# Performance work log

Hardware: AMD Instinct MI355X
Metric: run time of the kernel (lower is better)

Reference implementation:

```python
import jax, jax.numpy as jnp
import numpy as np

EPS = 1e-5      # numerical floor for degrees / std / attenuation
LEAK = 0.01     # LeakyReLU slope of mixing FCLayer
AVG_D = 3.3     # log(avg_degree + 1) from init_kwargs
BIG = 1e30      # masking constant for max/min aggregators


def setup_inputs() -> dict:
    key = jax.random.key(0)
    ks = jax.random.split(key, 12)
    B, N, Din, De, H = 8, 256, 128, 64, 128
    s = 0.05
    inp = {
        "input": jax.random.normal(ks[0], (B, N, Din), jnp.float32),
        "adj": (jax.random.uniform(ks[1], (B, N, N)) < 0.1).astype(jnp.float32),
        "adj_features": jax.random.normal(ks[2], (B, N, N, De), jnp.float32),
        "hidden": jnp.zeros((B * N, H), jnp.float32),
        "pre_W": jax.random.normal(ks[3], (2 * Din + De, Din), jnp.float32) * s,
        "pre_b": jnp.zeros((Din,), jnp.float32),
        "post_W": jax.random.normal(ks[4], (13 * Din, H), jnp.float32) * s,
        "post_b": jnp.zeros((H,), jnp.float32),
        "mix_W": jax.random.normal(ks[5], (H, H), jnp.float32) * s,
        "mix_b": jnp.zeros((H,), jnp.float32),
        "gru_Wih": jax.random.normal(ks[6], (3 * H, H), jnp.float32) * s,
        "gru_Whh": jax.random.normal(ks[7], (3 * H, H), jnp.float32) * s,
    }
    return inp


def reference(input, adj, adj_features, hidden, pre_W, pre_b, post_W, post_b,
              mix_W, mix_b, gru_Wih, gru_Whh):
    B, N, Din = input.shape
    H = mix_W.shape[1]
    # --- pretrans MLP over all pairs: Linear([h_i, h_j, e_ij]) ---
    # split the weight into blocks so we never materialize h_cat (B,N,N,2Din+De)
    Wi, Wj, We = pre_W[:Din], pre_W[Din:2 * Din], pre_W[2 * Din:]
    hi = input @ Wi            # (B,N,Din)
    hj = input @ Wj            # (B,N,Din)
    h_mod = (hi[:, :, None, :] + hj[:, None, :, :]
             + jnp.einsum('bije,ek->bijk', adj_features, We) + pre_b)  # (B,N,N,Din)
    # --- multi-aggregator masked reduction over source axis j ---
    deg = jnp.sum(adj, axis=2)                       # (B,N)
    degc = jnp.maximum(deg, EPS)[..., None]          # (B,N,1)
    s1 = jnp.einsum('bij,bijk->bik', adj, h_mod)
    s2 = jnp.einsum('bij,bijk->bik', adj, h_mod * h_mod)
    mean = s1 / degc
    var = jnp.maximum(s2 / degc - mean * mean, 0.0)
    std = jnp.sqrt(var + EPS)
    mask = adj[..., None] > 0
    has_nb = (deg > 0)[..., None]
    mx = jnp.where(has_nb, jnp.max(jnp.where(mask, h_mod, -BIG), axis=2), 0.0)
    mn = jnp.where(has_nb, jnp.min(jnp.where(mask, h_mod, BIG), axis=2), 0.0)
    m = jnp.concatenate([mean, mx, mn, std], axis=2)  # (B,N,4*Din)
    # --- scalers: identity, amplification, attenuation ---
    slog = (jnp.log(deg + 1.0) / AVG_D)[..., None]    # (B,N,1)
    m = jnp.concatenate([m, m * slog, m / (slog + EPS)], axis=2)  # (B,N,12*Din)
    # --- posttrans Linear + mixing FCLayer (LeakyReLU) ---
    m_cat = jnp.concatenate([input, m], axis=2)       # (B,N,13*Din)
    y = m_cat @ post_W + post_b                       # (B,N,H)
    y = y @ mix_W + mix_b
    y = jnp.where(y > 0, y, LEAK * y)
    # --- GRUCell (bias=False), torch gate order r,z,n ---
    x = y.reshape(B * N, H)
    gi = x @ gru_Wih.T
    gh = hidden @ gru_Whh.T
    r = jax.nn.sigmoid(gi[:, :H] + gh[:, :H])
    z = jax.nn.sigmoid(gi[:, H:2 * H] + gh[:, H:2 * H])
    n = jnp.tanh(gi[:, 2 * H:] + r * gh[:, 2 * H:])
    h_new = (1.0 - z) * n + z * hidden
    return h_new.reshape(B, N, H)
```

## Files before the change

kernel.cpp:

```cpp
#include <hip/hip_runtime.h>
#include <cstdint>
#include <cstddef>

#define EPSF 1e-5f
#define LEAKF 0.01f
#define AVGD 3.3f

static constexpr int Nn = 256, DIN = 128, DE = 64, Hn = 128;
static constexpr int BN = 2048;
static constexpr int CT = 1664;

typedef short bf16x8 __attribute__((ext_vector_type(8)));
typedef float f32x4  __attribute__((ext_vector_type(4)));
union BF8 { bf16x8 v; uint16_t u[8]; };

__device__ __forceinline__ float bf2f(uint16_t u) { return __uint_as_float(((uint32_t)u) << 16); }
__device__ __forceinline__ float bflo(uint32_t u)  { return __uint_as_float(u << 16); }
__device__ __forceinline__ uint16_t f2bf(float f) {
  uint32_t u = __float_as_uint(f);
  u += 0x7fffu + ((u >> 16) & 1u);
  return (uint16_t)(u >> 16);
}

__device__ __forceinline__ int detect_bf16(const uint32_t* w) {
  float lo = bflo(w[threadIdx.x & 63]);
  unsigned long long ok = __ballot(fabsf(lo) < 64.f);
  return ok == 0xFFFFFFFFFFFFFFFFull;
}
__device__ __forceinline__ float loadf(const void* p, size_t i, int isbf) {
  return isbf ? bf2f(((const uint16_t*)p)[i]) : ((const float*)p)[i];
}
__device__ __forceinline__ f32x4 mfma16(bf16x8 a, bf16x8 b, f32x4 c) {
  return __builtin_amdgcn_mfma_f32_16x16x32_bf16(a, b, c, 0, 0, 0);
}

__global__ __launch_bounds__(256) void k_prep(
    const void* __restrict__ input, const void* __restrict__ pre_W,
    const void* __restrict__ post_W, const void* __restrict__ mix_W,
    const void* __restrict__ Wih, const void* __restrict__ Whh,
    const void* __restrict__ hidden, const void* __restrict__ pre_b,
    uint16_t* __restrict__ preWTb, uint16_t* __restrict__ postTb,
    uint16_t* __restrict__ mixTb, uint16_t* __restrict__ Wihb,
    uint16_t* __restrict__ Whhb, uint16_t* __restrict__ hidb,
    uint16_t* __restrict__ Ab, float* __restrict__ hi, float* __restrict__ hj) {
  int isbf = detect_bf16((const uint32_t*)input);
  int b = blockIdx.x, tid = threadIdx.x;
  if (b < 264) {
    __shared__ float tile[32][33];
    const void* src; int R, C, t; uint16_t* bdst;
    if (b < 16)       { src = mix_W;  R = 128;  C = 128; t = b;       bdst = mixTb; }
    else if (b < 224) { src = post_W; R = 1664; C = 128; t = b - 16;  bdst = postTb; }
    else              { src = pre_W;  R = 320;  C = 128; t = b - 224; bdst = preWTb; }
    int bx = t & 3, by = t >> 2;
    int tx = tid & 31, ty = tid >> 5;
    int c0 = bx * 32, r0 = by * 32;
    #pragma unroll
    for (int dy = 0; dy < 32; dy += 8) {
      size_t idx = (size_t)(r0 + ty + dy) * C + (c0 + tx);
      tile[ty + dy][tx] = loadf(src, idx, isbf);
    }
    __syncthreads();
    #pragma unroll
    for (int dy = 0; dy < 32; dy += 8)
      bdst[(size_t)(c0 + ty + dy) * R + (r0 + tx)] = f2bf(tile[tx][ty + dy]);
  } else if (b < 440) {
    const void* src; uint16_t* dst; int base;
    if (b < 288)      { src = Wih;    dst = Wihb; base = (b - 264) * 2048; }
    else if (b < 312) { src = Whh;    dst = Whhb; base = (b - 288) * 2048; }
    else              { src = hidden; dst = hidb; base = (b - 312) * 2048; }
    int i = base + tid * 8;
    uint16_t v[8];
    if (isbf) *(uint4*)v = *(const uint4*)((const uint16_t*)src + i);
    else { const float* s = (const float*)src + i;
           #pragma unroll
           for (int e = 0; e < 8; e++) v[e] = f2bf(s[e]); }
    *(uint4*)(dst + i) = *(uint4*)v;
  } else if (b < 568) {
    int idx = (b - 440) * 2048 + tid * 8;
    int node = idx >> 7, col = idx & 127;
    uint16_t v[8];
    if (isbf) *(uint4*)v = *(const uint4*)((const uint16_t*)input + idx);
    else { const float* s = (const float*)input + idx;
           #pragma unroll
           for (int e = 0; e < 8; e++) v[e] = f2bf(s[e]); }
    *(uint4*)(Ab + (size_t)node * CT + col) = *(uint4*)v;
  } else {
    int lane = tid & 63, w = tid >> 6;
    int wg = (b - 568) * 4 + w;
    int rt = wg >> 4, nt = wg & 15;
    int ishj = nt >> 3, ct = nt & 7;
    int m16 = lane & 15, quad = lane >> 4;
    int col = ct * 16 + m16;
    int row = rt * 16 + m16;
    int kbase = ishj ? 128 : 0;
    f32x4 acc = {0.f, 0.f, 0.f, 0.f};
    #pragma unroll
    for (int kt = 0; kt < 4; kt++) {
      bf16x8 av;
      if (isbf) av = *(const bf16x8*)((const uint16_t*)input + (size_t)row * 128 + kt * 32 + quad * 8);
      else { const float* s = (const float*)input + (size_t)row * 128 + kt * 32 + quad * 8;
             BF8 t;
             #pragma unroll
             for (int e = 0; e < 8; e++) t.u[e] = f2bf(s[e]);
             av = t.v; }
      BF8 bb;
      #pragma unroll
      for (int j = 0; j < 8; j++) {
        size_t wi = (size_t)(kbase + kt * 32 + quad * 8 + j) * 128 + col;
        bb.u[j] = isbf ? ((const uint16_t*)pre_W)[wi] : f2bf(((const float*)pre_W)[wi]);
      }
      acc = mfma16(av, bb.v, acc);
    }
    float bias = ishj ? 0.f : loadf(pre_b, col, isbf);
    float* dst = ishj ? hj : hi;
    #pragma unroll
    for (int r = 0; r < 4; r++)
      dst[(size_t)(rt * 16 + quad * 4 + r) * 128 + col] = acc[r] + bias;
  }
}

__global__ __launch_bounds__(256) void k2_mfma(
    const void* __restrict__ input, const void* __restrict__ adj_raw,
    const void* __restrict__ af_raw,
    const float* __restrict__ hi, const float* __restrict__ hj,
    const uint16_t* __restrict__ preWTb, uint16_t* __restrict__ Ab) {
  __shared__ int nbr[Nn];
  __shared__ int wcnt[4];
  int isbf = detect_bf16((const uint32_t*)input);
  int bi = blockIdx.x, tid = threadIdx.x;
  int lane = tid & 63, w = tid >> 6;

  float a = loadf(adj_raw, (size_t)bi * Nn + tid, isbf);
  unsigned long long bm = __ballot(a > 0.f);
  int pre = __popcll(bm & ((1ull << lane) - 1ull));
  if (lane == 0) wcnt[w] = __popcll(bm);
  __syncthreads();
  int base = 0, cnt = 0;
  #pragma unroll
  for (int i = 0; i < 4; i++) { if (i < w) base += wcnt[i]; cnt += wcnt[i]; }
  if (a > 0.f) nbr[base + pre] = tid;
  __syncthreads();

  int m16 = lane & 15, quad = lane >> 4;
  int col0 = w * 32 + m16, col1 = col0 + 16;

  bf16x8 b00 = *(const bf16x8*)&preWTb[(size_t)col0 * 320 + 256 + quad * 8];
  bf16x8 b01 = *(const bf16x8*)&preWTb[(size_t)col0 * 320 + 288 + quad * 8];
  bf16x8 b10 = *(const bf16x8*)&preWTb[(size_t)col1 * 320 + 256 + quad * 8];
  bf16x8 b11 = *(const bf16x8*)&preWTb[(size_t)col1 * 320 + 288 + quad * 8];

  float base0 = hi[(size_t)bi * 128 + col0];
  float base1 = hi[(size_t)bi * 128 + col1];
  const float* hjb = &hj[(size_t)(bi & ~(Nn - 1)) * 128];

  float s1a = 0.f, s2a = 0.f, mxa = -1e30f, mna = 1e30f;
  float s1b = 0.f, s2b = 0.f, mxb = -1e30f, mnb = 1e30f;

  for (int ce = 0; ce < cnt; ce += 16) {
    int ei = ce + m16; if (ei >= cnt) ei = cnt - 1;
    int j = nbr[ei];
    bf16x8 a0, a1;
    if (isbf) {
      const uint16_t* ar = (const uint16_t*)af_raw + ((size_t)bi * Nn + j) * DE;
      a0 = *(const bf16x8*)(ar + quad * 8);
      a1 = *(const bf16x8*)(ar + 32 + quad * 8);
    } else {
      const float* ar = (const float*)af_raw + ((size_t)bi * Nn + j) * DE;
      BF8 t0, t1;
      #pragma unroll
      for (int e = 0; e < 8; e++) {
        t0.u[e] = f2bf(ar[quad * 8 + e]);
        t1.u[e] = f2bf(ar[32 + quad * 8 + e]);
      }
      a0 = t0.v; a1 = t1.v;
    }
    float hjv0[4], hjv1[4]; int vld[4];
    #pragma unroll
    for (int r = 0; r < 4; r++) {
      int e = ce + quad * 4 + r;
      vld[r] = (e < cnt);
      int jj = nbr[vld[r] ? e : (cnt - 1)];
      hjv0[r] = hjb[(size_t)jj * 128 + col0];
      hjv1[r] = hjb[(size_t)jj * 128 + col1];
    }
    f32x4 C0 = {0.f,0.f,0.f,0.f}, C1 = C0;
    C0 = mfma16(a0, b00, C0); C0 = mfma16(a1, b01, C0);
    C1 = mfma16(a0, b10, C1); C1 = mfma16(a1, b11, C1);
    #pragma unroll
    for (int r = 0; r < 4; r++) {
      float h0 = base0 + hjv0[r] + C0[r];
      float h1 = base1 + hjv1[r] + C1[r];
      if (vld[r]) {
        s1a += h0; s2a += h0 * h0; mxa = fmaxf(mxa, h0); mna = fminf(mna, h0);
        s1b += h1; s2b += h1 * h1; mxb = fmaxf(mxb, h1); mnb = fminf(mnb, h1);
      }
    }
  }
  #pragma unroll
  for (int off = 16; off <= 32; off <<= 1) {
    s1a += __shfl_xor(s1a, off); s2a += __shfl_xor(s2a, off);
    mxa = fmaxf(mxa, __shfl_xor(mxa, off)); mna = fminf(mna, __shfl_xor(mna, off));
    s1b += __shfl_xor(s1b, off); s2b += __shfl_xor(s2b, off);
    mxb = fmaxf(mxb, __shfl_xor(mxb, off)); mnb = fminf(mnb, __shfl_xor(mnb, off));
  }
  if (quad == 0) {
    float deg = (float)cnt, degc = fmaxf(deg, EPSF);
    float slog = logf(deg + 1.f) / AVGD;
    float inv  = 1.f / (slog + EPSF);
    uint16_t* mo = Ab + (size_t)bi * CT + 128;
    #pragma unroll
    for (int t = 0; t < 2; t++) {
      float s1 = t ? s1b : s1a, s2 = t ? s2b : s2a;
      float mx = t ? mxb : mxa, mn = t ? mnb : mna;
      int col = t ? col1 : col0;
      float mean = s1 / degc;
      float var  = fmaxf(s2 / degc - mean * mean, 0.f);
      float stdv = sqrtf(var + EPSF);
      if (cnt == 0) { mx = 0.f; mn = 0.f; }
      mo[0*128+col]  = f2bf(mean);        mo[1*128+col]  = f2bf(mx);
      mo[2*128+col]  = f2bf(mn);          mo[3*128+col]  = f2bf(stdv);
      mo[4*128+col]  = f2bf(mean * slog); mo[5*128+col]  = f2bf(mx * slog);
      mo[6*128+col]  = f2bf(mn * slog);   mo[7*128+col]  = f2bf(stdv * slog);
      mo[8*128+col]  = f2bf(mean * inv);  mo[9*128+col]  = f2bf(mx * inv);
      mo[10*128+col] = f2bf(mn * inv);    mo[11*128+col] = f2bf(stdv * inv);
    }
  }
}

__global__ __launch_bounds__(256) void k3a(
    const uint16_t* __restrict__ Ab, const uint16_t* __restrict__ postTb,
    const void* __restrict__ post_b, const void* __restrict__ input_flag,
    uint16_t* __restrict__ yb) {
  __shared__ float red[2][16][17];
  int isbf = detect_bf16((const uint32_t*)input_flag);
  int tid = threadIdx.x;
  int lane = tid & 63, w = tid >> 6;
  int wid = blockIdx.x * 4 + w;
  int tile = wid >> 1, kh = wid & 1, pair = w >> 1;
  int rt = tile >> 3, ct = tile & 7;
  int m16 = lane & 15, quad = lane >> 4;
  const uint16_t* ap = Ab     + (size_t)(rt * 16 + m16) * CT + kh * 832 + quad * 8;
  const uint16_t* bp = postTb + (size_t)(ct * 16 + m16) * CT + kh * 832 + quad * 8;
  f32x4 acc0 = {0.f,0.f,0.f,0.f}, acc1 = acc0;
  #pragma unroll 13
  for (int kt = 0; kt < 26; kt += 2) {
    acc0 = mfma16(*(const bf16x8*)(ap + kt * 32),      *(const bf16x8*)(bp + kt * 32),      acc0);
    acc1 = mfma16(*(const bf16x8*)(ap + kt * 32 + 32), *(const bf16x8*)(bp + kt * 32 + 32), acc1);
  }
  if (kh == 1) {
    #pragma unroll
    for (int r = 0; r < 4; r++) red[pair][quad * 4 + r][m16] = acc0[r] + acc1[r];
  }
  __syncthreads();
  if (kh == 0) {
    int col = ct * 16 + m16;
    float pb = loadf(post_b, col, isbf);
    #pragma unroll
    for (int r = 0; r < 4; r++)
      yb[(size_t)(rt * 16 + quad * 4 + r) * 128 + col] =
          f2bf(acc0[r] + acc1[r] + red[pair][quad * 4 + r][m16] + pb);
  }
}

__global__ __launch_bounds__(512) void k3b(
    const uint16_t* __restrict__ yb, const uint16_t* __restrict__ mixTb,
    const void* __restrict__ mix_b, const uint16_t* __restrict__ Wihb,
    const uint16_t* __restrict__ Whhb, const uint16_t* __restrict__ hidb,
    const void* __restrict__ input_flag, void* __restrict__ out) {
  constexpr int SX = 136;
  __shared__ __align__(16) uint16_t x_s[16 * SX];
  __shared__ __align__(16) uint16_t hid_s[16 * SX];
  int isbf = detect_bf16((const uint32_t*)input_flag);
  int tid = threadIdx.x;
  int n0 = blockIdx.x * 16;
  if (tid < 256) {
    int row = tid >> 4, c = (tid & 15) * 8;
    *(uint4*)&hid_s[row * SX + c] = *(const uint4*)&hidb[(size_t)(n0 + row) * 128 + c];
  }
  int lane = tid & 63, w = tid >> 6;
  int m16 = lane & 15, quad = lane >> 4;
  int col = w * 16 + m16;

  f32x4 acc = {0.f,0.f,0.f,0.f};
  const uint16_t* ya = yb    + (size_t)(n0 + m16) * 128 + quad * 8;
  const uint16_t* mb = mixTb + (size_t)col * 128 + quad * 8;
  #pragma unroll
  for (int kt = 0; kt < 4; kt++)
    acc = mfma16(*(const bf16x8*)(ya + kt * 32), *(const bf16x8*)(mb + kt * 32), acc);
  float mbias = loadf(mix_b, col, isbf);
  __syncthreads();
  #pragma unroll
  for (int r = 0; r < 4; r++) {
    float v = acc[r] + mbias; v = v > 0.f ? v : LEAKF * v;
    x_s[(quad * 4 + r) * SX + col] = f2bf(v);
  }
  __syncthreads();

  f32x4 gi[3], gh[3];
  #pragma unroll
  for (int q = 0; q < 3; q++) { gi[q] = {0.f,0.f,0.f,0.f}; gh[q] = {0.f,0.f,0.f,0.f}; }
  const uint16_t* xa = &x_s[m16 * SX + quad * 8];
  const uint16_t* ha = &hid_s[m16 * SX + quad * 8];
  #pragma unroll
  for (int kt = 0; kt < 4; kt++) {
    bf16x8 ax = *(const bf16x8*)(xa + kt * 32);
    bf16x8 ah = *(const bf16x8*)(ha + kt * 32);
    #pragma unroll
    for (int q = 0; q < 3; q++) {
      bf16x8 bi = *(const bf16x8*)&Wihb[(size_t)(q * 128 + col) * 128 + kt * 32 + quad * 8];
      bf16x8 bh = *(const bf16x8*)&Whhb[(size_t)(q * 128 + col) * 128 + kt * 32 + quad * 8];
      gi[q] = mfma16(ax, bi, gi[q]);
      gh[q] = mfma16(ah, bh, gh[q]);
    }
  }
  #pragma unroll
  for (int r = 0; r < 4; r++) {
    int row = quad * 4 + r;
    float rg = 1.f / (1.f + expf(-(gi[0][r] + gh[0][r])));
    float zg = 1.f / (1.f + expf(-(gi[1][r] + gh[1][r])));
    float ng = tanhf(gi[2][r] + rg * gh[2][r]);
    float hv = bf2f(hid_s[row * SX + col]);
    float res = (1.f - zg) * ng + zg * hv;
    size_t oi = (size_t)(n0 + row) * 128 + col;
    if (isbf) ((uint16_t*)out)[oi] = f2bf(res);
    else      ((float*)out)[oi]    = res;
  }
}

extern "C" void kernel_launch(void* const* d_in, const int* in_sizes, int n_in,
                              void* d_out, int out_size, void* d_ws, size_t ws_size,
                              hipStream_t stream) {
  const void* input  = d_in[0];
  const void* adj    = d_in[1];
  const void* af     = d_in[2];
  const void* hidden = d_in[3];
  const void* pre_W  = d_in[4];
  const void* pre_b  = d_in[5];
  const void* post_W = d_in[6];
  const void* post_b = d_in[7];
  const void* mix_W  = d_in[8];
  const void* mix_b  = d_in[9];
  const void* Wih    = d_in[10];
  const void* Whh    = d_in[11];

  float* ws = (float*)d_ws;
  float* hi = ws;
  float* hj = hi + 262144;
  uint16_t* Ab     = (uint16_t*)(hj + 262144);
  uint16_t* postTb = Ab + (size_t)BN * CT;
  uint16_t* mixTb  = postTb + 212992;
  uint16_t* preWTb = mixTb + 16384;
  uint16_t* Wihb   = preWTb + 40960;
  uint16_t* Whhb   = Wihb + 49152;
  uint16_t* hidb   = Whhb + 49152;
  uint16_t* yb     = hidb + 262144;

  k_prep<<<1080, 256, 0, stream>>>(input, pre_W, post_W, mix_W, Wih, Whh, hidden, pre_b,
                                   preWTb, postTb, mixTb, Wihb, Whhb, hidb, Ab, hi, hj);
  k2_mfma<<<BN, 256, 0, stream>>>(input, adj, af, hi, hj, preWTb, Ab);
  k3a<<<512, 256, 0, stream>>>(Ab, postTb, post_b, input, yb);
  k3b<<<128, 512, 0, stream>>>(yb, mixTb, mix_b, Wihb, Whhb, hidb, input, d_out);
}
```

Measured before the change: 236.0 us.

## Fold degree scalers into post-GEMM and fuse post, mix and GRU kernels

Only the four base aggregates (mean, max, min, std) are stored per node, along with the degree. The amplification and attenuation scalers are applied after the GEMM as per-row scalars on three partial accumulators (post_W blocks at offsets 128/640/1152). This shrinks the A matrix from 1664 to 640 columns and cuts the k2 writes. The separate post-transform, mixing and GRU kernels are merged into one kernel processing 8 nodes per block, which removes the yb round trip and one launch. In exchange, each 16-row MFMA tile is half-wasted with duplicated rows, and the fused kernel runs only 256 blocks.

Result: no change. 239.5 us (+1.5%).

```diff
diff --git a/kernel.cpp b/kernel.cpp
--- a/kernel.cpp
+++ b/kernel.cpp
@@ -8,7 +8,8 @@
 
 static constexpr int Nn = 256, DIN = 128, DE = 64, Hn = 128;
 static constexpr int BN = 2048;
-static constexpr int CT = 1664;
+static constexpr int CTA = 640;
+static constexpr int CTW = 1664;
 
 typedef short bf16x8 __attribute__((ext_vector_type(8)));
 typedef float f32x4  __attribute__((ext_vector_type(4)));
@@ -83,7 +84,7 @@
     else { const float* s = (const float*)input + idx;
            #pragma unroll
            for (int e = 0; e < 8; e++) v[e] = f2bf(s[e]); }
-    *(uint4*)(Ab + (size_t)node * CT + col) = *(uint4*)v;
+    *(uint4*)(Ab + (size_t)node * CTA + col) = *(uint4*)v;
   } else {
     int lane = tid & 63, w = tid >> 6;
     int wg = (b - 568) * 4 + w;
@@ -123,7 +124,8 @@
     const void* __restrict__ input, const void* __restrict__ adj_raw,
     const void* __restrict__ af_raw,
     const float* __restrict__ hi, const float* __restrict__ hj,
-    const uint16_t* __restrict__ preWTb, uint16_t* __restrict__ Ab) {
+    const uint16_t* __restrict__ preWTb, uint16_t* __restrict__ Ab,
+    float* __restrict__ degw) {
   __shared__ int nbr[Nn];
   __shared__ int wcnt[4];
   int isbf = detect_bf16((const uint32_t*)input);
@@ -203,11 +205,10 @@
     s1b += __shfl_xor(s1b, off); s2b += __shfl_xor(s2b, off);
     mxb = fmaxf(mxb, __shfl_xor(mxb, off)); mnb = fminf(mnb, __shfl_xor(mnb, off));
   }
+  if (tid == 0) degw[bi] = (float)cnt;
   if (quad == 0) {
-    float deg = (float)cnt, degc = fmaxf(deg, EPSF);
-    float slog = logf(deg + 1.f) / AVGD;
-    float inv  = 1.f / (slog + EPSF);
-    uint16_t* mo = Ab + (size_t)bi * CT + 128;
+    float degc = fmaxf((float)cnt, EPSF);
+    uint16_t* mo = Ab + (size_t)bi * CTA + 128;
     #pragma unroll
     for (int t = 0; t < 2; t++) {
       float s1 = t ? s1b : s1a, s2 = t ? s2b : s2a;
@@ -217,113 +218,128 @@
       float var  = fmaxf(s2 / degc - mean * mean, 0.f);
       float stdv = sqrtf(var + EPSF);
       if (cnt == 0) { mx = 0.f; mn = 0.f; }
-      mo[0*128+col]  = f2bf(mean);        mo[1*128+col]  = f2bf(mx);
-      mo[2*128+col]  = f2bf(mn);          mo[3*128+col]  = f2bf(stdv);
-      mo[4*128+col]  = f2bf(mean * slog); mo[5*128+col]  = f2bf(mx * slog);
-      mo[6*128+col]  = f2bf(mn * slog);   mo[7*128+col]  = f2bf(stdv * slog);
-      mo[8*128+col]  = f2bf(mean * inv);  mo[9*128+col]  = f2bf(mx * inv);
-      mo[10*128+col] = f2bf(mn * inv);    mo[11*128+col] = f2bf(stdv * inv);
-    }
-  }
-}
-
-__global__ __launch_bounds__(256) void k3a(
+      mo[0*128+col] = f2bf(mean); mo[1*128+col] = f2bf(mx);
+      mo[2*128+col] = f2bf(mn);   mo[3*128+col] = f2bf(stdv);
+    }
+  }
+}
+
+__global__ __launch_bounds__(256) void k3f(
     const uint16_t* __restrict__ Ab, const uint16_t* __restrict__ postTb,
-    const void* __restrict__ post_b, const void* __restrict__ input_flag,
-    uint16_t* __restrict__ yb) {
-  __shared__ float red[2][16][17];
+    const void* __restrict__ post_b, const uint16_t* __restrict__ mixTb,
+    const void* __restrict__ mix_b, const uint16_t* __restrict__ Wihb,
+    const uint16_t* __restrict__ Whhb, const uint16_t* __restrict__ hidb,
+    const float* __restrict__ degw, const void* __restrict__ input_flag,
+    void* __restrict__ out) {
+  constexpr int SX = 136;
+  __shared__ __align__(16) uint16_t y_s[8 * SX];
+  __shared__ __align__(16) uint16_t x_s[8 * SX];
+  __shared__ __align__(16) uint16_t hid_s[8 * SX];
   int isbf = detect_bf16((const uint32_t*)input_flag);
   int tid = threadIdx.x;
-  int lane = tid & 63, w = tid >> 6;
-  int wid = blockIdx.x * 4 + w;
-  int tile = wid >> 1, kh = wid & 1, pair = w >> 1;
-  int rt = tile >> 3, ct = tile & 7;
-  int m16 = lane & 15, quad = lane >> 4;
-  const uint16_t* ap = Ab     + (size_t)(rt * 16 + m16) * CT + kh * 832 + quad * 8;
-  const uint16_t* bp = postTb + (size_t)(ct * 16 + m16) * CT + kh * 832 + quad * 8;
-  f32x4 acc0 = {0.f,0.f,0.f,0.f}, acc1 = acc0;
-  #pragma unroll 13
-  for (int kt = 0; kt < 26; kt += 2) {
-    acc0 = mfma16(*(const bf16x8*)(ap + kt * 32),      *(const bf16x8*)(bp + kt * 32),      acc0);
-    acc1 = mfma16(*(const bf16x8*)(ap + kt * 32 + 32), *(const bf16x8*)(bp + kt * 32 + 32), acc1);
-  }
-  if (kh == 1) {
-    #pragma unroll
-    for (int r = 0; r < 4; r++) red[pair][quad * 4 + r][m16] = acc0[r] + acc1[r];
-  }
-  __syncthreads();
-  if (kh == 0) {
-    int col = ct * 16 + m16;
-    float pb = loadf(post_b, col, isbf);
-    #pragma unroll
-    for (int r = 0; r < 4; r++)
-      yb[(size_t)(rt * 16 + quad * 4 + r) * 128 + col] =
-          f2bf(acc0[r] + acc1[r] + red[pair][quad * 4 + r][m16] + pb);
-  }
-}
-
-__global__ __launch_bounds__(512) void k3b(
-    const uint16_t* __restrict__ yb, const uint16_t* __restrict__ mixTb,
-    const void* __restrict__ mix_b, const uint16_t* __restrict__ Wihb,
-    const uint16_t* __restrict__ Whhb, const uint16_t* __restrict__ hidb,
-    const void* __restrict__ input_flag, void* __restrict__ out) {
-  constexpr int SX = 136;
-  __shared__ __align__(16) uint16_t x_s[16 * SX];
-  __shared__ __align__(16) uint16_t hid_s[16 * SX];
-  int isbf = detect_bf16((const uint32_t*)input_flag);
-  int tid = threadIdx.x;
-  int n0 = blockIdx.x * 16;
-  if (tid < 256) {
+  int n0 = blockIdx.x * 8;
+  if (tid < 128) {
     int row = tid >> 4, c = (tid & 15) * 8;
     *(uint4*)&hid_s[row * SX + c] = *(const uint4*)&hidb[(size_t)(n0 + row) * 128 + c];
   }
   int lane = tid & 63, w = tid >> 6;
   int m16 = lane & 15, quad = lane >> 4;
-  int col = w * 16 + m16;
-
-  f32x4 acc = {0.f,0.f,0.f,0.f};
-  const uint16_t* ya = yb    + (size_t)(n0 + m16) * 128 + quad * 8;
-  const uint16_t* mb = mixTb + (size_t)col * 128 + quad * 8;
-  #pragma unroll
-  for (int kt = 0; kt < 4; kt++)
-    acc = mfma16(*(const bf16x8*)(ya + kt * 32), *(const bf16x8*)(mb + kt * 32), acc);
-  float mbias = loadf(mix_b, col, isbf);
+  const uint16_t* ap = Ab + (size_t)(n0 + (m16 & 7)) * CTA + quad * 8;
+  int col0 = (w * 2) * 16 + m16, col1 = (w * 2 + 1) * 16 + m16;
+  const uint16_t* bp0 = postTb + (size_t)col0 * CTW + quad * 8;
+  const uint16_t* bp1 = postTb + (size_t)col1 * CTW + quad * 8;
+
+  f32x4 aX0 = {0.f,0.f,0.f,0.f}, aX1 = aX0;
+  f32x4 a10 = aX0, a11 = aX0, a20 = aX0, a21 = aX0, a30 = aX0, a31 = aX0;
+  #pragma unroll
+  for (int kt = 0; kt < 4; kt++) {
+    bf16x8 a = *(const bf16x8*)(ap + kt * 32);
+    aX0 = mfma16(a, *(const bf16x8*)(bp0 + kt * 32), aX0);
+    aX1 = mfma16(a, *(const bf16x8*)(bp1 + kt * 32), aX1);
+  }
+  #pragma unroll 4
+  for (int kk = 0; kk < 16; kk++) {
+    bf16x8 a = *(const bf16x8*)(ap + 128 + kk * 32);
+    a10 = mfma16(a, *(const bf16x8*)(bp0 + 128  + kk * 32), a10);
+    a20 = mfma16(a, *(const bf16x8*)(bp0 + 640  + kk * 32), a20);
+    a30 = mfma16(a, *(const bf16x8*)(bp0 + 1152 + kk * 32), a30);
+    a11 = mfma16(a, *(const bf16x8*)(bp1 + 128  + kk * 32), a11);
+    a21 = mfma16(a, *(const bf16x8*)(bp1 + 640  + kk * 32), a21);
+    a31 = mfma16(a, *(const bf16x8*)(bp1 + 1152 + kk * 32), a31);
+  }
+  float pb0 = loadf(post_b, col0, isbf), pb1 = loadf(post_b, col1, isbf);
+  #pragma unroll
+  for (int r = 0; r < 4; r++) {
+    int row = quad * 4 + r;
+    if (row < 8) {
+      float deg = degw[n0 + row];
+      float slog = logf(deg + 1.f) / AVGD;
+      float inv  = 1.f / (slog + EPSF);
+      y_s[row * SX + col0] = f2bf(aX0[r] + a10[r] + slog * a20[r] + inv * a30[r] + pb0);
+      y_s[row * SX + col1] = f2bf(aX1[r] + a11[r] + slog * a21[r] + inv * a31[r] + pb1);
+    }
+  }
   __syncthreads();
+
+  const uint16_t* ya = &y_s[(m16 & 7) * SX + quad * 8];
+  const uint16_t* mb0 = mixTb + (size_t)col0 * 128 + quad * 8;
+  const uint16_t* mb1 = mixTb + (size_t)col1 * 128 + quad * 8;
+  f32x4 mm0 = {0.f,0.f,0.f,0.f}, mm1 = mm0;
+  #pragma unroll
+  for (int kt = 0; kt < 4; kt++) {
+    bf16x8 a = *(const bf16x8*)(ya + kt * 32);
+    mm0 = mfma16(a, *(const bf16x8*)(mb0 + kt * 32), mm0);
+    mm1 = mfma16(a, *(const bf16x8*)(mb1 + kt * 32), mm1);
+  }
+  float mbias0 = loadf(mix_b, col0, isbf), mbias1 = loadf(mix_b, col1, isbf);
   #pragma unroll
   for (int r = 0; r < 4; r++) {
-    float v = acc[r] + mbias; v = v > 0.f ? v : LEAKF * v;
-    x_s[(quad * 4 + r) * SX + col] = f2bf(v);
+    int row = quad * 4 + r;
+    if (row < 8) {
+      float v0 = mm0[r] + mbias0; v0 = v0 > 0.f ? v0 : LEAKF * v0;
+      float v1 = mm1[r] + mbias1; v1 = v1 > 0.f ? v1 : LEAKF * v1;
+      x_s[row * SX + col0] = f2bf(v0);
+      x_s[row * SX + col1] = f2bf(v1);
+    }
   }
   __syncthreads();
 
-  f32x4 gi[3], gh[3];
-  #pragma unroll
-  for (int q = 0; q < 3; q++) { gi[q] = {0.f,0.f,0.f,0.f}; gh[q] = {0.f,0.f,0.f,0.f}; }
-  const uint16_t* xa = &x_s[m16 * SX + quad * 8];
-  const uint16_t* ha = &hid_s[m16 * SX + quad * 8];
+  f32x4 gi[3][2], gh[3][2];
+  #pragma unroll
+  for (int q = 0; q < 3; q++)
+    #pragma unroll
+    for (int t = 0; t < 2; t++) { gi[q][t] = {0.f,0.f,0.f,0.f}; gh[q][t] = {0.f,0.f,0.f,0.f}; }
+  const uint16_t* xa = &x_s[(m16 & 7) * SX + quad * 8];
+  const uint16_t* ha = &hid_s[(m16 & 7) * SX + quad * 8];
   #pragma unroll
   for (int kt = 0; kt < 4; kt++) {
     bf16x8 ax = *(const bf16x8*)(xa + kt * 32);
     bf16x8 ah = *(const bf16x8*)(ha + kt * 32);
     #pragma unroll
     for (int q = 0; q < 3; q++) {
-      bf16x8 bi = *(const bf16x8*)&Wihb[(size_t)(q * 128 + col) * 128 + kt * 32 + quad * 8];
-      bf16x8 bh = *(const bf16x8*)&Whhb[(size_t)(q * 128 + col) * 128 + kt * 32 + quad * 8];
-      gi[q] = mfma16(ax, bi, gi[q]);
-      gh[q] = mfma16(ah, bh, gh[q]);
-    }
-  }
-  #pragma unroll
-  for (int r = 0; r < 4; r++) {
-    int row = quad * 4 + r;
-    float rg = 1.f / (1.f + expf(-(gi[0][r] + gh[0][r])));
-    float zg = 1.f / (1.f + expf(-(gi[1][r] + gh[1][r])));
-    float ng = tanhf(gi[2][r] + rg * gh[2][r]);
-    float hv = bf2f(hid_s[row * SX + col]);
-    float res = (1.f - zg) * ng + zg * hv;
-    size_t oi = (size_t)(n0 + row) * 128 + col;
-    if (isbf) ((uint16_t*)out)[oi] = f2bf(res);
-    else      ((float*)out)[oi]    = res;
+      gi[q][0] = mfma16(ax, *(const bf16x8*)&Wihb[(size_t)(q * 128 + col0) * 128 + kt * 32 + quad * 8], gi[q][0]);
+      gi[q][1] = mfma16(ax, *(const bf16x8*)&Wihb[(size_t)(q * 128 + col1) * 128 + kt * 32 + quad * 8], gi[q][1]);
+      gh[q][0] = mfma16(ah, *(const bf16x8*)&Whhb[(size_t)(q * 128 + col0) * 128 + kt * 32 + quad * 8], gh[q][0]);
+      gh[q][1] = mfma16(ah, *(const bf16x8*)&Whhb[(size_t)(q * 128 + col1) * 128 + kt * 32 + quad * 8], gh[q][1]);
+    }
+  }
+  #pragma unroll
+  for (int t = 0; t < 2; t++) {
+    int col = t ? col1 : col0;
+    #pragma unroll
+    for (int r = 0; r < 4; r++) {
+      int row = quad * 4 + r;
+      if (row < 8) {
+        float rg = 1.f / (1.f + expf(-(gi[0][t][r] + gh[0][t][r])));
+        float zg = 1.f / (1.f + expf(-(gi[1][t][r] + gh[1][t][r])));
+        float ng = tanhf(gi[2][t][r] + rg * gh[2][t][r]);
+        float hv = bf2f(hid_s[row * SX + col]);
+        float res = (1.f - zg) * ng + zg * hv;
+        size_t oi = (size_t)(n0 + row) * 128 + col;
+        if (isbf) ((uint16_t*)out)[oi] = f2bf(res);
+        else      ((float*)out)[oi]    = res;
+      }
+    }
   }
 }
 
@@ -344,20 +360,20 @@
   const void* Whh    = d_in[11];
 
   float* ws = (float*)d_ws;
-  float* hi = ws;
-  float* hj = hi + 262144;
-  uint16_t* Ab     = (uint16_t*)(hj + 262144);
-  uint16_t* postTb = Ab + (size_t)BN * CT;
+  float* hi   = ws;
+  float* hj   = hi + 262144;
+  float* degw = hj + 262144;
+  uint16_t* Ab     = (uint16_t*)(degw + 2048);
+  uint16_t* postTb = Ab + (size_t)BN * CTA;
   uint16_t* mixTb  = postTb + 212992;
   uint16_t* preWTb = mixTb + 16384;
   uint16_t* Wihb   = preWTb + 40960;
   uint16_t* Whhb   = Wihb + 49152;
   uint16_t* hidb   = Whhb + 49152;
-  uint16_t* yb     = hidb + 262144;
 
   k_prep<<<1080, 256, 0, stream>>>(input, pre_W, post_W, mix_W, Wih, Whh, hidden, pre_b,
                                    preWTb, postTb, mixTb, Wihb, Whhb, hidb, Ab, hi, hj);
-  k2_mfma<<<BN, 256, 0, stream>>>(input, adj, af, hi, hj, preWTb, Ab);
-  k3a<<<512, 256, 0, stream>>>(Ab, postTb, post_b, input, yb);
-  k3b<<<128, 512, 0, stream>>>(yb, mixTb, mix_b, Wihb, Whhb, hidb, input, d_out);
-}
+  k2_mfma<<<BN, 256, 0, stream>>>(input, adj, af, hi, hj, preWTb, Ab, degw);
+  k3f<<<256, 256, 0, stream>>>(Ab, postTb, post_b, mixTb, mix_b,
+                               Wihb, Whhb, hidb, degw, input, d_out);
+}
```
